# Optimization experiments

Hardware: AMD Instinct MI355X
Metric: run time of the kernel (lower is better)

Reference implementation:

```python
import jax, jax.numpy as jnp
import numpy as np

D_MODEL = 1024
D_FF = 2048        # SwiGLU hidden (first linear outputs 2*D_FF)
NUM_EXPERTS = 8
TOP_K = 2
BATCH, SEQ = 2, 2048


def setup_inputs() -> dict:
    key = jax.random.key(0)
    ks = jax.random.split(key, 5)
    s = 0.02
    x = jax.random.normal(ks[0], (BATCH, SEQ, D_MODEL), jnp.float32)
    Wr = jax.random.normal(ks[1], (D_MODEL, NUM_EXPERTS), jnp.float32) * s
    temp = jnp.ones((1,), jnp.float32)  # router_temp parameter
    W1 = jax.random.normal(ks[2], (NUM_EXPERTS, D_MODEL, 2 * D_FF), jnp.float32) * s
    b1 = jnp.zeros((NUM_EXPERTS, 2 * D_FF), jnp.float32)
    W2 = jax.random.normal(ks[3], (NUM_EXPERTS, D_FF, D_MODEL), jnp.float32) * s
    b2 = jnp.zeros((NUM_EXPERTS, D_MODEL), jnp.float32)
    return {"x": x, "Wr": Wr, "temp": temp, "W1": W1, "b1": b1, "W2": W2, "b2": b2}


def reference(x, Wr, temp, W1, b1, W2, b2):
    # Eval-mode forward: no router noise, dropout is identity.
    B, S, D = x.shape
    xf = x.reshape(-1, D)                       # [T, D], T = B*S
    logits = (xf @ Wr) / temp                   # [T, E]
    topw, topi = jax.lax.top_k(logits, TOP_K)   # [T, K]
    topw = jax.nn.softmax(topw, axis=-1)        # renormalized top-k weights
    out = jnp.zeros_like(xf)
    for e in range(NUM_EXPERTS):                # small fixed expert count
        h = xf @ W1[e] + b1[e]                  # [T, 2F]
        a, g = jnp.split(h, 2, axis=-1)         # SwiGLU: a * silu(g)
        y = (a * jax.nn.silu(g)) @ W2[e] + b2[e]  # [T, D]
        # combine weight for expert e (0 if not routed to e)
        we = jnp.sum(jnp.where(topi == e, topw, 0.0), axis=-1, keepdims=True)
        out = out + y * we
    return out.reshape(B, S, D)
```

## Files before the change

### kernel.cpp

```cpp
#include <hip/hip_runtime.h>
#include <hip/hip_bf16.h>
#include <math.h>


#define T_TOK  4096
#define DMODEL 1024
#define NEXP   8
#define FF     2048
#define FF2    4096

typedef __bf16 bf16_t;
typedef bf16_t bf16x8 __attribute__((ext_vector_type(8)));
typedef float  f32x4  __attribute__((ext_vector_type(4)));

__device__ __forceinline__ void gload_lds16(const void* g, void* l) {
  __builtin_amdgcn_global_load_lds((const __attribute__((address_space(1))) void*)g,
                                   (__attribute__((address_space(3))) void*)l, 16, 0, 0);
}

__global__ __launch_bounds__(256) void moe_router(
    const float* __restrict__ x, const float* __restrict__ Wr,
    const float* __restrict__ temp, const float* __restrict__ b2,
    bf16_t* __restrict__ xb, float* __restrict__ out,
    int* __restrict__ cnt, int* __restrict__ tok_list, float* __restrict__ w_list)
{
  __shared__ float sWr[DMODEL * NEXP];
  for (int i = threadIdx.x; i < DMODEL * NEXP; i += 256) sWr[i] = Wr[i];
  __syncthreads();

  int wave = threadIdx.x >> 6, lane = threadIdx.x & 63;
  int t = blockIdx.x * 4 + wave;
  const float* xr = x + (size_t)t * DMODEL;

  f32x4 acc0 = {0.f, 0.f, 0.f, 0.f}, acc1 = {0.f, 0.f, 0.f, 0.f};
  #pragma unroll
  for (int i = 0; i < 16; ++i) {
    int d = lane + 64 * i;
    float v = xr[d];
    xb[(size_t)t * DMODEL + d] = (bf16_t)v;
    const f32x4* wr = (const f32x4*)&sWr[d * NEXP];
    acc0 += v * wr[0];
    acc1 += v * wr[1];
  }
  #pragma unroll
  for (int off = 32; off; off >>= 1) {
    #pragma unroll
    for (int q = 0; q < 4; ++q) {
      acc0[q] += __shfl_down(acc0[q], off, 64);
      acc1[q] += __shfl_down(acc1[q], off, 64);
    }
  }
  int bi = 0, si = 0; float wb = 0.f, wsc = 0.f;
  if (lane == 0) {
    float invt = 1.f / temp[0];
    float lg[NEXP] = {acc0[0], acc0[1], acc0[2], acc0[3],
                      acc1[0], acc1[1], acc1[2], acc1[3]};
    float best = -3.4e38f, sec = -3.4e38f;
    #pragma unroll
    for (int e = 0; e < NEXP; ++e) {
      float l = lg[e] * invt;
      if (l > best)     { sec = best; si = bi; best = l; bi = e; }
      else if (l > sec) { sec = l; si = e; }
    }
    float ex = expf(sec - best);
    wb  = 1.f / (1.f + ex);
    wsc = ex  / (1.f + ex);
    int p0 = atomicAdd(&cnt[bi], 1);
    tok_list[bi * T_TOK + p0] = t; w_list[bi * T_TOK + p0] = wb;
    int p1 = atomicAdd(&cnt[si], 1);
    tok_list[si * T_TOK + p1] = t; w_list[si * T_TOK + p1] = wsc;
  }
  bi  = __shfl(bi, 0, 64);  si  = __shfl(si, 0, 64);
  wb  = __shfl(wb, 0, 64);  wsc = __shfl(wsc, 0, 64);
  const float* b2a = b2 + (size_t)bi * DMODEL;
  const float* b2b = b2 + (size_t)si * DMODEL;
  float* orow = out + (size_t)t * DMODEL;
  #pragma unroll
  for (int i = 0; i < 16; ++i) {
    int d = lane + 64 * i;
    orow[d] = wb * b2a[d] + wsc * b2b[d];
  }
}

__global__ void moe_prefix(const int* __restrict__ cnt, int* __restrict__ offs) {
  if (threadIdx.x == 0) {
    int s = 0;
    for (int e = 0; e < NEXP; ++e) { offs[e] = s; s += cnt[e]; }
    offs[NEXP] = s;
  }
}

__global__ __launch_bounds__(256) void tcast64(
    const float* __restrict__ in, bf16_t* __restrict__ outp, int R, int C)
{
  __shared__ float tile[64][65];
  const float* inp = in + (size_t)blockIdx.z * R * C;
  bf16_t* op = outp + (size_t)blockIdx.z * R * C;
  int c0 = blockIdx.x * 64, r0 = blockIdx.y * 64;
  int tx = threadIdx.x & 63, ty = threadIdx.x >> 6;
  #pragma unroll
  for (int j = 0; j < 64; j += 4)
    tile[ty + j][tx] = inp[(size_t)(r0 + ty + j) * C + c0 + tx];
  __syncthreads();
  #pragma unroll
  for (int j = 0; j < 64; j += 4)
    op[(size_t)(c0 + ty + j) * R + r0 + tx] = (bf16_t)tile[tx][ty + j];
}

__global__ __launch_bounds__(256) void moe_gemm1(
    const bf16_t* __restrict__ xb, const bf16_t* __restrict__ W1t,
    const float* __restrict__ b1, const int* __restrict__ cnt,
    const int* __restrict__ offs, const int* __restrict__ tok_list,
    const float* __restrict__ w_list, bf16_t* __restrict__ U,
    int e_base, long estride)
{
  int e = e_base + blockIdx.z;
  int count = cnt[e];
  int m0 = blockIdx.y * 128;
  if (m0 >= count) return;
  int nt = blockIdx.x;
  const bf16_t* W1e = W1t + (size_t)blockIdx.z * estride;

  __shared__ bf16_t As[128 * 64];
  __shared__ bf16_t Bs[128 * 64];
  __shared__ int   stok[128];
  __shared__ float sw[128];
  int tid = threadIdx.x;
  if (tid < 128) {
    int m = m0 + tid;
    stok[tid] = (m < count) ? tok_list[e * T_TOK + m] : 0;
    sw[tid]   = (m < count) ? w_list[e * T_TOK + m] : 0.f;
  }
  __syncthreads();

  int wave = tid >> 6, lane = tid & 63;
  int quad = lane >> 4, l16 = lane & 15;
  int rsub = lane >> 3;
  int swz  = (lane & 7) ^ rsub;

  size_t asrc[4]; const bf16_t* bsrc[4];
  bf16_t* aldst[4]; bf16_t* bldst[4];
  #pragma unroll
  for (int s = 0; s < 4; ++s) {
    int inst = wave * 4 + s;
    int row = inst * 8 + rsub;
    asrc[s] = (size_t)stok[row] * DMODEL + swz * 8;
    int grow = (row < 64) ? (nt * 64 + row) : (FF + nt * 64 + (row - 64));
    bsrc[s] = W1e + (size_t)grow * DMODEL + swz * 8;
    aldst[s] = As + inst * 512;
    bldst[s] = Bs + inst * 512;
  }

  f32x4 acc[2][8];
  #pragma unroll
  for (int i = 0; i < 2; ++i)
    #pragma unroll
    for (int j = 0; j < 8; ++j) acc[i][j] = (f32x4){0.f, 0.f, 0.f, 0.f};

  for (int k0 = 0; k0 < DMODEL; k0 += 64) {
    __syncthreads();
    #pragma unroll
    for (int s = 0; s < 4; ++s) {
      gload_lds16(xb + asrc[s] + k0, aldst[s]);
      gload_lds16(bsrc[s] + k0, bldst[s]);
    }
    __syncthreads();
    #pragma unroll
    for (int kh = 0; kh < 2; ++kh) {
      int so = ((kh * 4 + quad) ^ (l16 & 7)) * 8;
      bf16x8 a0 = *(const bf16x8*)&As[(wave * 32      + l16) * 64 + so];
      bf16x8 a1 = *(const bf16x8*)&As[(wave * 32 + 16 + l16) * 64 + so];
      #pragma unroll
      for (int j = 0; j < 8; ++j) {
        bf16x8 b = *(const bf16x8*)&Bs[(j * 16 + l16) * 64 + so];
        acc[0][j] = __builtin_amdgcn_mfma_f32_16x16x32_bf16(a0, b, acc[0][j], 0, 0, 0);
        acc[1][j] = __builtin_amdgcn_mfma_f32_16x16x32_bf16(a1, b, acc[1][j], 0, 0, 0);
      }
    }
  }

  int uoff = offs[e];
  const float* b1e = b1 + (size_t)e * FF2;
  #pragma unroll
  for (int j = 0; j < 4; ++j) {
    int f = nt * 64 + j * 16 + l16;
    float ba = b1e[f];
    float bg = b1e[FF + f];
    #pragma unroll
    for (int i = 0; i < 2; ++i) {
      f32x4 av = acc[i][j];
      f32x4 gv = acc[i][j + 4];
      #pragma unroll
      for (int r = 0; r < 4; ++r) {
        int m = wave * 32 + i * 16 + quad * 4 + r;
        if (m0 + m < count) {
          float aa = av[r] + ba;
          float gg = gv[r] + bg;
          float u = sw[m] * aa * gg / (1.f + __expf(-gg));
          U[(size_t)(uoff + m0 + m) * FF + f] = (bf16_t)u;
        }
      }
    }
  }
}

__global__ __launch_bounds__(256) void moe_gemm2(
    const bf16_t* __restrict__ U, const bf16_t* __restrict__ W2t,
    const int* __restrict__ cnt, const int* __restrict__ offs,
    const int* __restrict__ tok_list, float* __restrict__ out,
    int e_base, long estride)
{
  int e = e_base + blockIdx.z;
  int count = cnt[e];
  int m0 = blockIdx.y * 128;
  if (m0 >= count) return;
  int n0 = blockIdx.x * 128;
  const bf16_t* W2e = W2t + (size_t)blockIdx.z * estride;

  __shared__ bf16_t As[128 * 64];
  __shared__ bf16_t Bs[128 * 64];
  __shared__ int stok[128];
  int tid = threadIdx.x;
  if (tid < 128) {
    int m = m0 + tid;
    stok[tid] = (m < count) ? tok_list[e * T_TOK + m] : 0;
  }
  int wave = tid >> 6, lane = tid & 63;
  int quad = lane >> 4, l16 = lane & 15;
  int rsub = lane >> 3;
  int swz  = (lane & 7) ^ rsub;
  int uoff = offs[e];

  const bf16_t* asrc[4]; const bf16_t* bsrc[4];
  bf16_t* aldst[4]; bf16_t* bldst[4];
  #pragma unroll
  for (int s = 0; s < 4; ++s) {
    int inst = wave * 4 + s;
    int row = inst * 8 + rsub;
    asrc[s] = U   + (size_t)(uoff + m0 + row) * FF + swz * 8;
    bsrc[s] = W2e + (size_t)(n0 + row)        * FF + swz * 8;
    aldst[s] = As + inst * 512;
    bldst[s] = Bs + inst * 512;
  }

  f32x4 acc[2][8];
  #pragma unroll
  for (int i = 0; i < 2; ++i)
    #pragma unroll
    for (int j = 0; j < 8; ++j) acc[i][j] = (f32x4){0.f, 0.f, 0.f, 0.f};

  for (int k0 = 0; k0 < FF; k0 += 64) {
    __syncthreads();
    #pragma unroll
    for (int s = 0; s < 4; ++s) {
      gload_lds16(asrc[s] + k0, aldst[s]);
      gload_lds16(bsrc[s] + k0, bldst[s]);
    }
    __syncthreads();
    #pragma unroll
    for (int kh = 0; kh < 2; ++kh) {
      int so = ((kh * 4 + quad) ^ (l16 & 7)) * 8;
      bf16x8 a0 = *(const bf16x8*)&As[(wave * 32      + l16) * 64 + so];
      bf16x8 a1 = *(const bf16x8*)&As[(wave * 32 + 16 + l16) * 64 + so];
      #pragma unroll
      for (int j = 0; j < 8; ++j) {
        bf16x8 b = *(const bf16x8*)&Bs[(j * 16 + l16) * 64 + so];
        acc[0][j] = __builtin_amdgcn_mfma_f32_16x16x32_bf16(a0, b, acc[0][j], 0, 0, 0);
        acc[1][j] = __builtin_amdgcn_mfma_f32_16x16x32_bf16(a1, b, acc[1][j], 0, 0, 0);
      }
    }
  }

  #pragma unroll
  for (int j = 0; j < 8; ++j) {
    int n = n0 + j * 16 + l16;
    #pragma unroll
    for (int i = 0; i < 2; ++i) {
      f32x4 av = acc[i][j];
      #pragma unroll
      for (int r = 0; r < 4; ++r) {
        int m = wave * 32 + i * 16 + quad * 4 + r;
        if (m0 + m < count)
          atomicAdd(&out[(size_t)stok[m] * DMODEL + n], av[r]);
      }
    }
  }
}

extern "C" void kernel_launch(void* const* d_in, const int* in_sizes, int n_in,
                              void* d_out, int out_size, void* d_ws, size_t ws_size,
                              hipStream_t stream)
{
  const float* x    = (const float*)d_in[0];
  const float* Wr   = (const float*)d_in[1];
  const float* temp = (const float*)d_in[2];
  const float* W1   = (const float*)d_in[3];
  const float* b1   = (const float*)d_in[4];
  const float* W2   = (const float*)d_in[5];
  const float* b2   = (const float*)d_in[6];
  float* out = (float*)d_out;

  char* ws = (char*)d_ws;
  size_t off = 0;
  auto alloc = [&](size_t b) { void* p = ws + off; off += (b + 255) & ~(size_t)255; return p; };
  bf16_t* xb  = (bf16_t*)alloc((size_t)T_TOK * DMODEL * 2);
  bf16_t* U   = (bf16_t*)alloc((size_t)(2 * T_TOK + 128) * FF * 2);
  int*   cnt  = (int*)alloc(256);
  int*   offs = (int*)alloc(256);
  int*   tok  = (int*)alloc((size_t)NEXP * T_TOK * 4);
  float* wl   = (float*)alloc((size_t)NEXP * T_TOK * 4);
  size_t base = off;
  const size_t W1T_FULL = (size_t)NEXP * FF2 * DMODEL * 2;
  const size_t W2T_FULL = (size_t)NEXP * DMODEL * FF * 2;
  bool batched = (ws_size >= base + W1T_FULL + W2T_FULL);

  hipMemsetAsync(cnt, 0, NEXP * sizeof(int), stream);
  moe_router<<<dim3(T_TOK / 4), dim3(256), 0, stream>>>(x, Wr, temp, b2, xb, out, cnt, tok, wl);
  moe_prefix<<<dim3(1), dim3(64), 0, stream>>>(cnt, offs);

  if (batched) {
    bf16_t* W1t = (bf16_t*)alloc(W1T_FULL);
    bf16_t* W2t = (bf16_t*)alloc(W2T_FULL);
    tcast64<<<dim3(FF2 / 64, DMODEL / 64, NEXP), dim3(256), 0, stream>>>(W1, W1t, DMODEL, FF2);
    tcast64<<<dim3(DMODEL / 64, FF / 64, NEXP), dim3(256), 0, stream>>>(W2, W2t, FF, DMODEL);
    moe_gemm1<<<dim3(FF / 64, T_TOK / 128, NEXP), dim3(256), 0, stream>>>(
        xb, W1t, b1, cnt, offs, tok, wl, U, 0, (long)FF2 * DMODEL);
    moe_gemm2<<<dim3(DMODEL / 128, T_TOK / 128, NEXP), dim3(256), 0, stream>>>(
        U, W2t, cnt, offs, tok, out, 0, (long)DMODEL * FF);
  } else {
    bf16_t* W1t = (bf16_t*)alloc((size_t)FF2 * DMODEL * 2);
    bf16_t* W2t = (bf16_t*)alloc((size_t)DMODEL * FF * 2);
    for (int e = 0; e < NEXP; ++e) {
      tcast64<<<dim3(FF2 / 64, DMODEL / 64, 1), dim3(256), 0, stream>>>(
          W1 + (size_t)e * DMODEL * FF2, W1t, DMODEL, FF2);
      moe_gemm1<<<dim3(FF / 64, T_TOK / 128, 1), dim3(256), 0, stream>>>(
          xb, W1t, b1, cnt, offs, tok, wl, U, e, 0);
    }
    for (int e = 0; e < NEXP; ++e) {
      tcast64<<<dim3(DMODEL / 64, FF / 64, 1), dim3(256), 0, stream>>>(
          W2 + (size_t)e * FF * DMODEL, W2t, FF, DMODEL);
      moe_gemm2<<<dim3(DMODEL / 128, T_TOK / 128, 1), dim3(256), 0, stream>>>(
          U, W2t, cnt, offs, tok, out, e, 0);
    }
  }
}
```

Before: 582.0 us.

## Replace gemm2 scatter atomics with dense output plus combine kernel; vectorize weight transpose-cast

```diff
diff --git a/kernel.cpp b/kernel.cpp
--- a/kernel.cpp
+++ b/kernel.cpp
@@ -20,9 +20,10 @@
 
 __global__ __launch_bounds__(256) void moe_router(
     const float* __restrict__ x, const float* __restrict__ Wr,
-    const float* __restrict__ temp, const float* __restrict__ b2,
-    bf16_t* __restrict__ xb, float* __restrict__ out,
-    int* __restrict__ cnt, int* __restrict__ tok_list, float* __restrict__ w_list)
+    const float* __restrict__ temp,
+    bf16_t* __restrict__ xb,
+    int* __restrict__ cnt, int* __restrict__ tok_list, float* __restrict__ w_list,
+    int* __restrict__ slot)
 {
   __shared__ float sWr[DMODEL * NEXP];
   for (int i = threadIdx.x; i < DMODEL * NEXP; i += 256) sWr[i] = Wr[i];
@@ -50,11 +51,11 @@
       acc1[q] += __shfl_down(acc1[q], off, 64);
     }
   }
-  int bi = 0, si = 0; float wb = 0.f, wsc = 0.f;
   if (lane == 0) {
     float invt = 1.f / temp[0];
     float lg[NEXP] = {acc0[0], acc0[1], acc0[2], acc0[3],
                       acc1[0], acc1[1], acc1[2], acc1[3]};
+    int bi = 0, si = 0;
     float best = -3.4e38f, sec = -3.4e38f;
     #pragma unroll
     for (int e = 0; e < NEXP; ++e) {
@@ -63,22 +64,14 @@
       else if (l > sec) { sec = l; si = e; }
     }
     float ex = expf(sec - best);
-    wb  = 1.f / (1.f + ex);
-    wsc = ex  / (1.f + ex);
+    float wb  = 1.f / (1.f + ex);
+    float wsc = ex  / (1.f + ex);
     int p0 = atomicAdd(&cnt[bi], 1);
     tok_list[bi * T_TOK + p0] = t; w_list[bi * T_TOK + p0] = wb;
     int p1 = atomicAdd(&cnt[si], 1);
     tok_list[si * T_TOK + p1] = t; w_list[si * T_TOK + p1] = wsc;
-  }
-  bi  = __shfl(bi, 0, 64);  si  = __shfl(si, 0, 64);
-  wb  = __shfl(wb, 0, 64);  wsc = __shfl(wsc, 0, 64);
-  const float* b2a = b2 + (size_t)bi * DMODEL;
-  const float* b2b = b2 + (size_t)si * DMODEL;
-  float* orow = out + (size_t)t * DMODEL;
-  #pragma unroll
-  for (int i = 0; i < 16; ++i) {
-    int d = lane + 64 * i;
-    orow[d] = wb * b2a[d] + wsc * b2b[d];
+    slot[2 * t]     = bi * T_TOK + p0;
+    slot[2 * t + 1] = si * T_TOK + p1;
   }
 }
 
@@ -90,21 +83,33 @@
   }
 }
 
-__global__ __launch_bounds__(256) void tcast64(
+__global__ __launch_bounds__(256) void tcast_fast(
     const float* __restrict__ in, bf16_t* __restrict__ outp, int R, int C)
 {
   __shared__ float tile[64][65];
   const float* inp = in + (size_t)blockIdx.z * R * C;
   bf16_t* op = outp + (size_t)blockIdx.z * R * C;
   int c0 = blockIdx.x * 64, r0 = blockIdx.y * 64;
-  int tx = threadIdx.x & 63, ty = threadIdx.x >> 6;
-  #pragma unroll
-  for (int j = 0; j < 64; j += 4)
-    tile[ty + j][tx] = inp[(size_t)(r0 + ty + j) * C + c0 + tx];
+  int tid = threadIdx.x;
+  int lr = tid >> 4;
+  int lc4 = (tid & 15) * 4;
+  #pragma unroll
+  for (int p = 0; p < 4; ++p) {
+    int r = p * 16 + lr;
+    const float4 v = *(const float4*)&inp[(size_t)(r0 + r) * C + c0 + lc4];
+    tile[r][lc4 + 0] = v.x; tile[r][lc4 + 1] = v.y;
+    tile[r][lc4 + 2] = v.z; tile[r][lc4 + 3] = v.w;
+  }
   __syncthreads();
-  #pragma unroll
-  for (int j = 0; j < 64; j += 4)
-    op[(size_t)(c0 + ty + j) * R + r0 + tx] = (bf16_t)tile[tx][ty + j];
+  int rr8 = (tid & 7) * 8;
+  #pragma unroll
+  for (int it = 0; it < 2; ++it) {
+    int cc = (tid >> 3) + it * 32;
+    bf16x8 o;
+    #pragma unroll
+    for (int j = 0; j < 8; ++j) o[j] = (bf16_t)tile[rr8 + j][cc];
+    *(bf16x8*)&op[(size_t)(c0 + cc) * R + r0 + rr8] = o;
+  }
 }
 
 __global__ __launch_bounds__(256) void moe_gemm1(
@@ -207,7 +212,7 @@
 __global__ __launch_bounds__(256) void moe_gemm2(
     const bf16_t* __restrict__ U, const bf16_t* __restrict__ W2t,
     const int* __restrict__ cnt, const int* __restrict__ offs,
-    const int* __restrict__ tok_list, float* __restrict__ out,
+    float* __restrict__ Y,
     int e_base, long estride)
 {
   int e = e_base + blockIdx.z;
@@ -219,12 +224,7 @@
 
   __shared__ bf16_t As[128 * 64];
   __shared__ bf16_t Bs[128 * 64];
-  __shared__ int stok[128];
   int tid = threadIdx.x;
-  if (tid < 128) {
-    int m = m0 + tid;
-    stok[tid] = (m < count) ? tok_list[e * T_TOK + m] : 0;
-  }
   int wave = tid >> 6, lane = tid & 63;
   int quad = lane >> 4, l16 = lane & 15;
   int rsub = lane >> 3;
@@ -281,10 +281,29 @@
       for (int r = 0; r < 4; ++r) {
         int m = wave * 32 + i * 16 + quad * 4 + r;
         if (m0 + m < count)
-          atomicAdd(&out[(size_t)stok[m] * DMODEL + n], av[r]);
+          Y[(size_t)(uoff + m0 + m) * DMODEL + n] = av[r];
       }
     }
   }
+}
+
+__global__ __launch_bounds__(256) void moe_combine(
+    const float* __restrict__ Y, const float* __restrict__ b2,
+    const int* __restrict__ slot, const float* __restrict__ w_list,
+    const int* __restrict__ offs, float* __restrict__ out)
+{
+  int t = blockIdx.x;
+  int v0 = slot[2 * t], v1 = slot[2 * t + 1];
+  int e0 = v0 >> 12, p0 = v0 & (T_TOK - 1);
+  int e1 = v1 >> 12, p1 = v1 & (T_TOK - 1);
+  int r0 = offs[e0] + p0, r1 = offs[e1] + p1;
+  float w0 = w_list[v0], w1 = w_list[v1];
+  int d = threadIdx.x * 4;
+  f32x4 y0 = *(const f32x4*)&Y[(size_t)r0 * DMODEL + d];
+  f32x4 y1 = *(const f32x4*)&Y[(size_t)r1 * DMODEL + d];
+  f32x4 c0 = *(const f32x4*)&b2[(size_t)e0 * DMODEL + d];
+  f32x4 c1 = *(const f32x4*)&b2[(size_t)e1 * DMODEL + d];
+  *(f32x4*)&out[(size_t)t * DMODEL + d] = y0 + y1 + w0 * c0 + w1 * c1;
 }
 
 extern "C" void kernel_launch(void* const* d_in, const int* in_sizes, int n_in,
@@ -305,42 +324,45 @@
   auto alloc = [&](size_t b) { void* p = ws + off; off += (b + 255) & ~(size_t)255; return p; };
   bf16_t* xb  = (bf16_t*)alloc((size_t)T_TOK * DMODEL * 2);
   bf16_t* U   = (bf16_t*)alloc((size_t)(2 * T_TOK + 128) * FF * 2);
+  float*  Y   = (float*)alloc((size_t)(2 * T_TOK) * DMODEL * 4);
   int*   cnt  = (int*)alloc(256);
   int*   offs = (int*)alloc(256);
   int*   tok  = (int*)alloc((size_t)NEXP * T_TOK * 4);
   float* wl   = (float*)alloc((size_t)NEXP * T_TOK * 4);
+  int*   slot = (int*)alloc((size_t)2 * T_TOK * 4);
   size_t base = off;
   const size_t W1T_FULL = (size_t)NEXP * FF2 * DMODEL * 2;
   const size_t W2T_FULL = (size_t)NEXP * DMODEL * FF * 2;
   bool batched = (ws_size >= base + W1T_FULL + W2T_FULL);
 
   hipMemsetAsync(cnt, 0, NEXP * sizeof(int), stream);
-  moe_router<<<dim3(T_TOK / 4), dim3(256), 0, stream>>>(x, Wr, temp, b2, xb, out, cnt, tok, wl);
+  moe_router<<<dim3(T_TOK / 4), dim3(256), 0, stream>>>(x, Wr, temp, xb, cnt, tok, wl, slot);
   moe_prefix<<<dim3(1), dim3(64), 0, stream>>>(cnt, offs);
 
   if (batched) {
     bf16_t* W1t = (bf16_t*)alloc(W1T_FULL);
     bf16_t* W2t = (bf16_t*)alloc(W2T_FULL);
-    tcast64<<<dim3(FF2 / 64, DMODEL / 64, NEXP), dim3(256), 0, stream>>>(W1, W1t, DMODEL, FF2);
-    tcast64<<<dim3(DMODEL / 64, FF / 64, NEXP), dim3(256), 0, stream>>>(W2, W2t, FF, DMODEL);
+    tcast_fast<<<dim3(FF2 / 64, DMODEL / 64, NEXP), dim3(256), 0, stream>>>(W1, W1t, DMODEL, FF2);
+    tcast_fast<<<dim3(DMODEL / 64, FF / 64, NEXP), dim3(256), 0, stream>>>(W2, W2t, FF, DMODEL);
     moe_gemm1<<<dim3(FF / 64, T_TOK / 128, NEXP), dim3(256), 0, stream>>>(
         xb, W1t, b1, cnt, offs, tok, wl, U, 0, (long)FF2 * DMODEL);
     moe_gemm2<<<dim3(DMODEL / 128, T_TOK / 128, NEXP), dim3(256), 0, stream>>>(
-        U, W2t, cnt, offs, tok, out, 0, (long)DMODEL * FF);
+        U, W2t, cnt, offs, Y, 0, (long)DMODEL * FF);
   } else {
     bf16_t* W1t = (bf16_t*)alloc((size_t)FF2 * DMODEL * 2);
     bf16_t* W2t = (bf16_t*)alloc((size_t)DMODEL * FF * 2);
     for (int e = 0; e < NEXP; ++e) {
-      tcast64<<<dim3(FF2 / 64, DMODEL / 64, 1), dim3(256), 0, stream>>>(
+      tcast_fast<<<dim3(FF2 / 64, DMODEL / 64, 1), dim3(256), 0, stream>>>(
           W1 + (size_t)e * DMODEL * FF2, W1t, DMODEL, FF2);
       moe_gemm1<<<dim3(FF / 64, T_TOK / 128, 1), dim3(256), 0, stream>>>(
           xb, W1t, b1, cnt, offs, tok, wl, U, e, 0);
     }
     for (int e = 0; e < NEXP; ++e) {
-      tcast64<<<dim3(DMODEL / 64, FF / 64, 1), dim3(256), 0, stream>>>(
+      tcast_fast<<<dim3(DMODEL / 64, FF / 64, 1), dim3(256), 0, stream>>>(
           W2 + (size_t)e * FF * DMODEL, W2t, FF, DMODEL);
       moe_gemm2<<<dim3(DMODEL / 128, T_TOK / 128, 1), dim3(256), 0, stream>>>(
-          U, W2t, cnt, offs, tok, out, e, 0);
-    }
-  }
-}
+          U, W2t, cnt, offs, Y, e, 0);
+    }
+  }
+  moe_combine<<<dim3(T_TOK), dim3(256), 0, stream>>>(Y, b2, slot, wl, offs, out);
+}
```

Measured after the change: 538.9 us. 7.4% less time.
